# Kernel optimization log

Measured on AMD Instinct MI355X. Metric: run time of the kernel, lower is better.

The kernel has to match this reference:

```python
import jax, jax.numpy as jnp
import numpy as np

K = 16          # neighbors per center (init arg K)
EPS = 1e-5      # layernorm epsilon


def _dcconv(pos, ch, W, b, n_in, n_out, resnet_in=None, Wres=None, bres=None):
    """KNN-gathered distance-contained conv.
    pos: [B, n_in, 3], ch: [B, n_in, Cin], W: [Cout, K, Cin].
    Selects n_out strided centers, gathers K nearest neighbors, convolves.
    """
    stride = n_in // n_out
    idx = jnp.arange(n_out) * stride                      # static center indices
    cpos = pos[:, idx]                                    # [B, n_out, 3]
    # squared pairwise distances centers -> all points: [B, n_out, n_in]
    d2 = jnp.sum((cpos[:, :, None, :] - pos[:, None, :, :]) ** 2, axis=-1)
    _, knn = jax.lax.top_k(-d2, K)                        # [B, n_out, K]
    gathered = jax.vmap(lambda c, i: c[i])(ch, knn)       # [B, n_out, K, Cin]
    out = jnp.einsum('bnkc,okc->bno', gathered, W) + b    # [B, n_out, Cout]
    if resnet_in is None:
        res = ch[:, idx] @ Wres + bres                    # project skip to Cout
    else:
        res = resnet_in[:, idx]                           # downsample carried skip
    return cpos, out, res


def _layernorm(x, g, b):
    mu = jnp.mean(x, axis=-1, keepdims=True)
    var = jnp.var(x, axis=-1, keepdims=True)
    return (x - mu) * jax.lax.rsqrt(var + EPS) * g + b


def setup_inputs() -> dict:
    key = jax.random.key(0)
    ks = jax.random.split(key, 8)
    B, N, Cin, Cout = 2, 8192, 64, 128
    s1 = (2.0 / (K * Cin)) ** 0.5
    s2 = (2.0 / (K * Cout)) ** 0.5
    return {
        'position_matrix': jax.random.normal(ks[0], (B, N, 3), jnp.float32),
        'channel_matrix': jax.random.normal(ks[1], (B, N, Cin), jnp.float32),
        'W1': jax.random.normal(ks[2], (Cout, K, Cin), jnp.float32) * s1,
        'b1': jnp.full((Cout,), 0.01, jnp.float32),
        'Wres': jax.random.normal(ks[3], (Cin, Cout), jnp.float32) * (2.0 / Cin) ** 0.5,
        'bres': jnp.full((Cout,), 0.01, jnp.float32),
        'W2': jax.random.normal(ks[4], (Cout, K, Cout), jnp.float32) * s2,
        'b2': jnp.full((Cout,), 0.01, jnp.float32),
        'g1': jnp.ones((Cout,), jnp.float32),
        'be1': jnp.full((Cout,), 0.01, jnp.float32),
        'g2': jnp.ones((Cout,), jnp.float32),
        'be2': jnp.full((Cout,), 0.01, jnp.float32),
        'n0': 8192, 'n1': 4096, 'n2': 2048,
    }


def reference(position_matrix, channel_matrix, W1, b1, Wres, bres, W2, b2,
              g1, be1, g2, be2, n0, n1, n2):
    pos, ch, res = _dcconv(position_matrix, channel_matrix, W1, b1, n0, n1,
                           None, Wres, bres)
    ch = jax.nn.silu(_layernorm(ch, g1, be1))   # dropout=identity (eval)
    pos, ch, res = _dcconv(pos, ch, W2, b2, n1, n2, resnet_in=res)
    ch = jax.nn.silu(_layernorm(ch, g2, be2))   # dropout=identity (eval)
    ch = ch + res                               # residual add
    return pos, ch
```

## Files before the change

### kernel.cpp

```cpp
#include <hip/hip_runtime.h>
#include <cstdint>
#include <cstddef>

using u16 = unsigned short;
using u32 = unsigned int;
using u64 = unsigned long long;

typedef short bf16x8 __attribute__((ext_vector_type(8)));
typedef float f32x4 __attribute__((ext_vector_type(4)));

constexpr int BATCH = 2;
constexpr int N0 = 8192;
constexpr int N1 = 4096;
constexpr int N2 = 2048;
constexpr int COUT = 128;
constexpr int KNB = 16;

__device__ __forceinline__ float bf2f(u16 v) { return __uint_as_float(((u32)v) << 16); }
__device__ __forceinline__ u16 f2bf(float f) {
    u32 u = __float_as_uint(f);
    return (u16)((u + 0x7fffu + ((u >> 16) & 1u)) >> 16);
}
__device__ __forceinline__ void cvt8(const float* __restrict__ src, u16* __restrict__ dst, int e) {
    float t0[8];
    *(float4*)t0 = *(const float4*)(src + e);
    *(float4*)(t0 + 4) = *(const float4*)(src + e + 4);
    u16 o[8];
#pragma unroll
    for (int q = 0; q < 8; ++q) o[q] = f2bf(t0[q]);
    *(uint4*)(dst + e) = *(uint4*)o;
}

__device__ __forceinline__ float dist2s(float cx, float cy, float cz,
                                        float px, float py, float pz) {
#pragma clang fp contract(off)
    float dx = cx - px;
    float dy = cy - py;
    float dz = cz - pz;
    float s = dx * dx;
    s = s + dy * dy;
    s = s + dz * dz;
    return s;
}

template <int CTRL>
__device__ __forceinline__ u64 dpp64(u64 v) {
    int lo = (int)(u32)v, hi = (int)(u32)(v >> 32);
    int plo = __builtin_amdgcn_update_dpp(0, lo, CTRL, 0xF, 0xF, true);
    int phi = __builtin_amdgcn_update_dpp(0, hi, CTRL, 0xF, 0xF, true);
    return (((u64)(u32)phi) << 32) | (u32)plo;
}
__device__ __forceinline__ u64 dpp_prev_u64(u64 v) { return dpp64<0x111>(v); }

__device__ __forceinline__ void knn_scan(const float* __restrict__ P, int pstride,
                                         int c0row, int c1row, int cnt,
                                         int lane, u64& rk0, u64& rk1) {
    const float* c0p = P + (size_t)c0row * pstride;
    const float* c1p = P + (size_t)c1row * pstride;
    float c0x = c0p[0], c0y = c0p[1], c0z = c0p[2];
    float c1x = c1p[0], c1y = c1p[1], c1z = c1p[2];

    u64 key0, key1;
    {
        const float* pp = P + (size_t)lane * pstride;
        float px = pp[0], py = pp[1], pz = pp[2];
        u64 k0 = (((u64)__float_as_uint(dist2s(c0x, c0y, c0z, px, py, pz))) << 32) | (u32)lane;
        u64 k1 = (((u64)__float_as_uint(dist2s(c1x, c1y, c1z, px, py, pz))) << 32) | (u32)lane;
#pragma unroll
        for (int kk = 2; kk <= 64; kk <<= 1)
#pragma unroll
            for (int jj = kk >> 1; jj > 0; jj >>= 1) {
                u64 o0, o1;
                if (jj == 1)      { o0 = dpp64<0xB1>(k0);  o1 = dpp64<0xB1>(k1); }
                else if (jj == 2) { o0 = dpp64<0x4E>(k0);  o1 = dpp64<0x4E>(k1); }
                else if (jj == 8) { o0 = dpp64<0x128>(k0); o1 = dpp64<0x128>(k1); }
                else              { o0 = __shfl_xor(k0, jj, 64); o1 = __shfl_xor(k1, jj, 64); }
                bool keepmin = (((lane & jj) == 0) == ((lane & kk) == 0));
                k0 = keepmin ? ((o0 < k0) ? o0 : k0) : ((o0 > k0) ? o0 : k0);
                k1 = keepmin ? ((o1 < k1) ? o1 : k1) : ((o1 > k1) ? o1 : k1);
            }
        key0 = k0; key1 = k1;
    }
    u32 cut0 = __shfl((u32)(key0 >> 32), 15, 64);
    u32 cut1 = __shfl((u32)(key1 >> 32), 15, 64);

    {
        const float* pp = P + (size_t)(64 + lane) * pstride;
        float px = pp[0], py = pp[1], pz = pp[2];
        u32 d0 = __float_as_uint(dist2s(c0x, c0y, c0z, px, py, pz));
        u32 d1 = __float_as_uint(dist2s(c1x, c1y, c1z, px, py, pz));
        u64 ball0 = __ballot(d0 <= cut0);
        u64 ball1 = __ballot(d1 <= cut1);
        bool any0 = ball0 != 0, any1 = ball1 != 0;
        while (ball0 | ball1) {
            if (ball0) {
                int src = __ffsll((unsigned long long)ball0) - 1;
                ball0 &= ball0 - 1;
                u64 nk = (((u64)__shfl(d0, src, 64)) << 32) | (u32)(64 + src);
                u64 prev = dpp_prev_u64(key0);
                key0 = (nk < key0) ? ((nk < prev) ? prev : nk) : key0;
            }
            if (ball1) {
                int src = __ffsll((unsigned long long)ball1) - 1;
                ball1 &= ball1 - 1;
                u64 nk = (((u64)__shfl(d1, src, 64)) << 32) | (u32)(64 + src);
                u64 prev = dpp_prev_u64(key1);
                key1 = (nk < key1) ? ((nk < prev) ? prev : nk) : key1;
            }
        }
        if (any0) cut0 = __shfl((u32)(key0 >> 32), 15, 64);
        if (any1) cut1 = __shfl((u32)(key1 >> 32), 15, 64);
    }

    int nstep = (cnt - 128) >> 7;
    const float* pa = P + (size_t)(128 + 2 * lane) * pstride;
    float ax = pa[0], ay = pa[1], az = pa[2];
    float bx = pa[pstride], by = pa[pstride + 1], bz = pa[pstride + 2];
    for (int s = 0; s < nstep; ++s) {
        float cax = ax, cay = ay, caz = az, cbx = bx, cby = by, cbz = bz;
        int nxt = (s + 1 < nstep) ? (s + 1) : s;
        const float* pn = P + (size_t)(128 + (nxt << 7) + 2 * lane) * pstride;
        ax = pn[0]; ay = pn[1]; az = pn[2];
        bx = pn[pstride]; by = pn[pstride + 1]; bz = pn[pstride + 2];
        int sb = 128 + (s << 7);
        u32 da0 = __float_as_uint(dist2s(c0x, c0y, c0z, cax, cay, caz));
        u32 da1 = __float_as_uint(dist2s(c1x, c1y, c1z, cax, cay, caz));
        u32 db0 = __float_as_uint(dist2s(c0x, c0y, c0z, cbx, cby, cbz));
        u32 db1 = __float_as_uint(dist2s(c1x, c1y, c1z, cbx, cby, cbz));
        u64 ba0 = __ballot(da0 <= cut0);
        u64 bb0 = __ballot(db0 <= cut0);
        u64 ba1 = __ballot(da1 <= cut1);
        u64 bb1 = __ballot(db1 <= cut1);
        bool any0 = (ba0 | bb0) != 0, any1 = (ba1 | bb1) != 0;
        while (ba0 | bb0 | ba1 | bb1) {
            if (ba0) {
                int src = __ffsll((unsigned long long)ba0) - 1;
                ba0 &= ba0 - 1;
                u64 nk = (((u64)__shfl(da0, src, 64)) << 32) | (u32)(sb + 2 * src);
                u64 prev = dpp_prev_u64(key0);
                key0 = (nk < key0) ? ((nk < prev) ? prev : nk) : key0;
            }
            if (ba1) {
                int src = __ffsll((unsigned long long)ba1) - 1;
                ba1 &= ba1 - 1;
                u64 nk = (((u64)__shfl(da1, src, 64)) << 32) | (u32)(sb + 2 * src);
                u64 prev = dpp_prev_u64(key1);
                key1 = (nk < key1) ? ((nk < prev) ? prev : nk) : key1;
            }
            if (bb0) {
                int src = __ffsll((unsigned long long)bb0) - 1;
                bb0 &= bb0 - 1;
                u64 nk = (((u64)__shfl(db0, src, 64)) << 32) | (u32)(sb + 2 * src + 1);
                u64 prev = dpp_prev_u64(key0);
                key0 = (nk < key0) ? ((nk < prev) ? prev : nk) : key0;
            }
            if (bb1) {
                int src = __ffsll((unsigned long long)bb1) - 1;
                bb1 &= bb1 - 1;
                u64 nk = (((u64)__shfl(db1, src, 64)) << 32) | (u32)(sb + 2 * src + 1);
                u64 prev = dpp_prev_u64(key1);
                key1 = (nk < key1) ? ((nk < prev) ? prev : nk) : key1;
            }
        }
        if (any0) cut0 = __shfl((u32)(key0 >> 32), 15, 64);
        if (any1) cut1 = __shfl((u32)(key1 >> 32), 15, 64);
    }
    rk0 = key0; rk1 = key1;
}

__global__ __launch_bounds__(256)
void knn_prep_kernel(const float* __restrict__ pos0, const float* __restrict__ ch0,
                     const float* __restrict__ W1, const float* __restrict__ W2,
                     const float* __restrict__ Wres,
                     int* __restrict__ knn1, int* __restrict__ knn2,
                     u16* __restrict__ ch0b, u16* __restrict__ W1b,
                     u16* __restrict__ W2b, u16* __restrict__ Wresb,
                     float* __restrict__ pos_out) {
    int blk = blockIdx.x, tid = threadIdx.x;
    int w = tid >> 6, lane = tid & 63;
    if (blk < 1024) {
        int wave = blk * 4 + w;
        int batch = wave >> 11, pj = wave & 2047;
        const float* P = pos0 + (size_t)batch * N0 * 3;
        u64 key0, key1;
        knn_scan(P, 3, 4 * pj, 4 * pj + 2, N0, lane, key0, key1);
        if (lane < 16) {
            knn1[((size_t)(batch * N1 + 2 * pj)) * KNB + lane] = (int)(u32)key0;
            knn1[((size_t)(batch * N1 + 2 * pj + 1)) * KNB + lane] = (int)(u32)key1;
        }
    } else if (blk < 1536) {
        int wave = (blk - 1024) * 4 + w;
        int batch = wave >> 10, pj = wave & 1023;
        const float* P = pos0 + (size_t)batch * N0 * 3;
        u64 key0, key1;
        knn_scan(P, 6, 4 * pj, 4 * pj + 2, N1, lane, key0, key1);
        if (lane < 16) {
            knn2[((size_t)(batch * N2 + 2 * pj)) * KNB + lane] = (int)(u32)key0;
            knn2[((size_t)(batch * N2 + 2 * pj + 1)) * KNB + lane] = (int)(u32)key1;
        }
    } else if (blk < 2048) {
        cvt8(ch0, ch0b, ((blk - 1536) * 256 + tid) * 8);
    } else if (blk < 2112) {
        cvt8(W1, W1b, ((blk - 2048) * 256 + tid) * 8);
    } else if (blk < 2240) {
        cvt8(W2, W2b, ((blk - 2112) * 256 + tid) * 8);
    } else if (blk < 2272) {
        int t = (blk - 2240) * 256 + tid;
        int o = t >> 6, c = t & 63;
        Wresb[o * 64 + c] = f2bf(Wres[(size_t)c * COUT + o]);
    } else {
        int t = (blk - 2272) * 256 + tid;
        int b = t >> 11, r = t & 2047;
        const float* s = pos0 + ((size_t)(b * N0 + r * 4)) * 3;
        float* d = pos_out + ((size_t)(b * N2 + r)) * 3;
        d[0] = s[0]; d[1] = s[1]; d[2] = s[2];
    }
}

__global__ __launch_bounds__(256)
void conv1_kernel(const u16* __restrict__ ch0b, const int* __restrict__ knn1,
                  const u16* __restrict__ W1b, const u16* __restrict__ Wresb,
                  const float* __restrict__ b1, const float* __restrict__ bres,
                  const float* __restrict__ g1, const float* __restrict__ be1,
                  u16* __restrict__ ch1b, u16* __restrict__ res1b) {
    __shared__ u16 As[16][72];
    __shared__ u16 Ws[128][72];
    __shared__ int knnr[16][16];
    __shared__ float red[16][4][2];
    __shared__ float cb[128], cg[128], cbe[128], cbr[128];

    int tid = threadIdx.x;
    int blk = blockIdx.x;
    int b = blk >> 8, g = blk & 255;
    int jbase = g * 16;

    if (tid < 128) { cb[tid] = b1[tid]; cg[tid] = g1[tid]; cbe[tid] = be1[tid]; cbr[tid] = bres[tid]; }
    {
        int r = tid >> 4, k = tid & 15;
        knnr[r][k] = knn1[((size_t)(b * N1 + jbase + r)) * KNB + k];
    }
    __syncthreads();

    int w = tid >> 6, lane = tid & 63, quad = lane >> 4, l15 = lane & 15;
    int wcol = w * 32;
    int ar = tid >> 4, ap = tid & 15;
    int wn = tid >> 1, wh = tid & 1;

    f32x4 acc[2] = {{0,0,0,0},{0,0,0,0}};
    f32x4 racc[2] = {{0,0,0,0},{0,0,0,0}};

    uint2 aR = *((const uint2*)(ch0b + ((size_t)(b * N0 + knnr[ar][0])) * 64) + ap);
    uint4 wR[4];
    {
        const uint4* s4 = (const uint4*)(W1b + (size_t)wn * 1024 + wh * 32);
        wR[0] = s4[0]; wR[1] = s4[1]; wR[2] = s4[2]; wR[3] = s4[3];
    }
    for (int kn = 0; kn < 17; ++kn) {
        *(uint2*)&As[ar][ap * 4] = aR;
        uint4* d4 = (uint4*)&Ws[wn][wh * 32];
        d4[0] = wR[0]; d4[1] = wR[1]; d4[2] = wR[2]; d4[3] = wR[3];
        __syncthreads();
        if (kn < 16) {
            int nidx = (kn < 15) ? knnr[ar][kn + 1] : 2 * (jbase + ar);
            aR = *((const uint2*)(ch0b + ((size_t)(b * N0 + nidx)) * 64) + ap);
            const uint4* s4 = (kn < 15)
                ? (const uint4*)(W1b + (size_t)wn * 1024 + (kn + 1) * 64 + wh * 32)
                : (const uint4*)(Wresb + (size_t)wn * 64 + wh * 32);
            wR[0] = s4[0]; wR[1] = s4[1]; wR[2] = s4[2]; wR[3] = s4[3];
        }
        if (kn < 16) {
#pragma unroll
            for (int ks = 0; ks < 2; ++ks) {
                bf16x8 af = *(const bf16x8*)&As[l15][ks * 32 + quad * 8];
#pragma unroll
                for (int nt = 0; nt < 2; ++nt) {
                    bf16x8 bfr = *(const bf16x8*)&Ws[wcol + nt * 16 + l15][ks * 32 + quad * 8];
                    acc[nt] = __builtin_amdgcn_mfma_f32_16x16x32_bf16(af, bfr, acc[nt], 0, 0, 0);
                }
            }
        } else {
#pragma unroll
            for (int ks = 0; ks < 2; ++ks) {
                bf16x8 af = *(const bf16x8*)&As[l15][ks * 32 + quad * 8];
#pragma unroll
                for (int nt = 0; nt < 2; ++nt) {
                    bf16x8 bfr = *(const bf16x8*)&Ws[wcol + nt * 16 + l15][ks * 32 + quad * 8];
                    racc[nt] = __builtin_amdgcn_mfma_f32_16x16x32_bf16(af, bfr, racc[nt], 0, 0, 0);
                }
            }
        }
        __syncthreads();
    }

    float x[2][4], s[4] = {0,0,0,0}, ss[4] = {0,0,0,0};
#pragma unroll
    for (int reg = 0; reg < 4; ++reg)
#pragma unroll
        for (int nt = 0; nt < 2; ++nt) {
            int col = wcol + nt * 16 + l15;
            float v = acc[nt][reg] + cb[col];
            x[nt][reg] = v;
            s[reg] += v; ss[reg] += v * v;
        }
#pragma unroll
    for (int m = 1; m < 16; m <<= 1)
#pragma unroll
        for (int reg = 0; reg < 4; ++reg) {
            s[reg] += __shfl_xor(s[reg], m, 64);
            ss[reg] += __shfl_xor(ss[reg], m, 64);
        }
    if (l15 == 0) {
#pragma unroll
        for (int reg = 0; reg < 4; ++reg) {
            red[quad * 4 + reg][w][0] = s[reg];
            red[quad * 4 + reg][w][1] = ss[reg];
        }
    }
    __syncthreads();
    float mu[4], rs[4];
#pragma unroll
    for (int reg = 0; reg < 4; ++reg) {
        int row = quad * 4 + reg;
        float S = red[row][0][0] + red[row][1][0] + red[row][2][0] + red[row][3][0];
        float SS = red[row][0][1] + red[row][1][1] + red[row][2][1] + red[row][3][1];
        mu[reg] = S * (1.f / 128.f);
        float var = fmaxf(SS * (1.f / 128.f) - mu[reg] * mu[reg], 0.f);
        rs[reg] = 1.f / sqrtf(var + 1e-5f);
    }
#pragma unroll
    for (int nt = 0; nt < 2; ++nt)
#pragma unroll
        for (int reg = 0; reg < 4; ++reg) {
            int col = wcol + nt * 16 + l15;
            int row = quad * 4 + reg;
            size_t off = ((size_t)(b * N1 + jbase + row)) * COUT + col;
            float y = (x[nt][reg] - mu[reg]) * rs[reg] * cg[col] + cbe[col];
            ch1b[off] = f2bf(y / (1.f + __expf(-y)));
            res1b[off] = f2bf(racc[nt][reg] + cbr[col]);
        }
}

__global__ __launch_bounds__(512)
void conv2_kernel(const u16* __restrict__ ch1b, const int* __restrict__ knn2,
                  const u16* __restrict__ W2b, const float* __restrict__ b2,
                  const float* __restrict__ g2, const float* __restrict__ be2,
                  const u16* __restrict__ res1b, float* __restrict__ ch_out) {
    __shared__ u16 As[16][136];
    __shared__ u16 Ws[128][136];
    __shared__ int knnr[16][16];
    __shared__ float red[16][8][2];
    __shared__ float cb[128], cg[128], cbe[128];

    int tid = threadIdx.x;
    int b = blockIdx.x >> 7, g = blockIdx.x & 127;
    int ibase = g * 16;

    if (tid < 128) { cb[tid] = b2[tid]; cg[tid] = g2[tid]; cbe[tid] = be2[tid]; }
    if (tid < 256) {
        int r = tid >> 4, k = tid & 15;
        knnr[r][k] = knn2[((size_t)(b * N2 + ibase + r)) * KNB + k];
    }
    __syncthreads();

    int w = tid >> 6, lane = tid & 63, quad = lane >> 4, l15 = lane & 15;
    int wcol = w * 16;
    int ar = tid >> 5, ap = tid & 31;
    int wn = tid >> 2, wq = tid & 3;

    f32x4 acc = {0, 0, 0, 0};

    uint2 aR = *((const uint2*)(ch1b + ((size_t)(b * N1 + knnr[ar][0])) * COUT) + ap);
    uint4 wR[4];
    {
        const uint4* s4 = (const uint4*)(W2b + (size_t)wn * 2048 + wq * 32);
        wR[0] = s4[0]; wR[1] = s4[1]; wR[2] = s4[2]; wR[3] = s4[3];
    }
    for (int kn = 0; kn < 16; ++kn) {
        *(uint2*)&As[ar][ap * 4] = aR;
        uint4* d4 = (uint4*)&Ws[wn][wq * 32];
        d4[0] = wR[0]; d4[1] = wR[1]; d4[2] = wR[2]; d4[3] = wR[3];
        __syncthreads();
        if (kn < 15) {
            aR = *((const uint2*)(ch1b + ((size_t)(b * N1 + knnr[ar][kn + 1])) * COUT) + ap);
            const uint4* s4 = (const uint4*)(W2b + (size_t)wn * 2048 + (kn + 1) * 128 + wq * 32);
            wR[0] = s4[0]; wR[1] = s4[1]; wR[2] = s4[2]; wR[3] = s4[3];
        }
#pragma unroll
        for (int ks = 0; ks < 4; ++ks) {
            bf16x8 af = *(const bf16x8*)&As[l15][ks * 32 + quad * 8];
            bf16x8 bfr = *(const bf16x8*)&Ws[wcol + l15][ks * 32 + quad * 8];
            acc = __builtin_amdgcn_mfma_f32_16x16x32_bf16(af, bfr, acc, 0, 0, 0);
        }
        __syncthreads();
    }

    float x[4], s[4], ss[4];
#pragma unroll
    for (int reg = 0; reg < 4; ++reg) {
        int col = wcol + l15;
        float v = acc[reg] + cb[col];
        x[reg] = v; s[reg] = v; ss[reg] = v * v;
    }
#pragma unroll
    for (int m = 1; m < 16; m <<= 1)
#pragma unroll
        for (int reg = 0; reg < 4; ++reg) {
            s[reg] += __shfl_xor(s[reg], m, 64);
            ss[reg] += __shfl_xor(ss[reg], m, 64);
        }
    if (l15 == 0) {
#pragma unroll
        for (int reg = 0; reg < 4; ++reg) {
            red[quad * 4 + reg][w][0] = s[reg];
            red[quad * 4 + reg][w][1] = ss[reg];
        }
    }
    __syncthreads();
#pragma unroll
    for (int reg = 0; reg < 4; ++reg) {
        int row = quad * 4 + reg;
        float S = 0.f, SS = 0.f;
#pragma unroll
        for (int t = 0; t < 8; ++t) { S += red[row][t][0]; SS += red[row][t][1]; }
        float mu = S * (1.f / 128.f);
        float var = fmaxf(SS * (1.f / 128.f) - mu * mu, 0.f);
        float rs = 1.f / sqrtf(var + 1e-5f);
        int col = wcol + l15;
        int i = ibase + row;
        float y = (x[reg] - mu) * rs * cg[col] + cbe[col];
        float sl = y / (1.f + __expf(-y));
        float rv = bf2f(res1b[((size_t)(b * N1 + 2 * i)) * COUT + col]);
        ch_out[((size_t)(b * N2 + i)) * COUT + col] = sl + rv;
    }
}

extern "C" void kernel_launch(void* const* d_in, const int* in_sizes, int n_in,
                              void* d_out, int out_size, void* d_ws, size_t ws_size,
                              hipStream_t stream) {
    const float* pos0 = (const float*)d_in[0];
    const float* ch0  = (const float*)d_in[1];
    const float* W1   = (const float*)d_in[2];
    const float* b1   = (const float*)d_in[3];
    const float* Wres = (const float*)d_in[4];
    const float* bres = (const float*)d_in[5];
    const float* W2   = (const float*)d_in[6];
    const float* b2   = (const float*)d_in[7];
    const float* g1   = (const float*)d_in[8];
    const float* be1  = (const float*)d_in[9];
    const float* g2   = (const float*)d_in[10];
    const float* be2  = (const float*)d_in[11];
    float* out = (float*)d_out;

    char* ws = (char*)d_ws;
    int*  knn1  = (int*)(ws);
    int*  knn2  = (int*)(ws + 524288);
    u16*  ch0b  = (u16*)(ws + 786432);
    u16*  W1b   = (u16*)(ws + 2883584);
    u16*  W2b   = (u16*)(ws + 3145728);
    u16*  Wresb = (u16*)(ws + 3670016);
    u16*  ch1b  = (u16*)(ws + 3686400);
    u16*  res1b = (u16*)(ws + 5783552);

    float* pos_out = out;
    float* ch_out  = out + 12288;

    knn_prep_kernel<<<2288, 256, 0, stream>>>(pos0, ch0, W1, W2, Wres,
                                              knn1, knn2, ch0b, W1b, W2b, Wresb, pos_out);
    conv1_kernel<<<512, 256, 0, stream>>>(ch0b, knn1, W1b, Wresb, b1, bres, g1, be1, ch1b, res1b);
    conv2_kernel<<<256, 512, 0, stream>>>(ch1b, knn2, W2b, b2, g2, be2, res1b, ch_out);
}
```

Before: 225.0 us.

## Move second KNN search into conv1 launch and use readlane for broadcasts

The second-level KNN search moves out of the prep kernel and into the conv1 kernel as extra blocks, so it overlaps with the first convolution instead of extending the prep kernel's long tail. Inside the scan, wave-uniform broadcasts switch from __shfl (LDS bpermute) to readlane, the point stride becomes a template parameter, and the conditional cut refresh becomes unconditional. This spreads KNN work across two launches but makes the conv1 launch heterogeneous, which can affect scheduling and occupancy.

```diff
diff --git a/kernel.cpp b/kernel.cpp
--- a/kernel.cpp
+++ b/kernel.cpp
@@ -9,7 +9,6 @@
 typedef short bf16x8 __attribute__((ext_vector_type(8)));
 typedef float f32x4 __attribute__((ext_vector_type(4)));
 
-constexpr int BATCH = 2;
 constexpr int N0 = 8192;
 constexpr int N1 = 4096;
 constexpr int N2 = 2048;
@@ -52,17 +51,22 @@
 }
 __device__ __forceinline__ u64 dpp_prev_u64(u64 v) { return dpp64<0x111>(v); }
 
-__device__ __forceinline__ void knn_scan(const float* __restrict__ P, int pstride,
+__device__ __forceinline__ u32 rdlane(u32 v, int l) {
+    return (u32)__builtin_amdgcn_readlane((int)v, l);
+}
+
+template <int PSTRIDE>
+__device__ __forceinline__ void knn_scan(const float* __restrict__ P,
                                          int c0row, int c1row, int cnt,
                                          int lane, u64& rk0, u64& rk1) {
-    const float* c0p = P + (size_t)c0row * pstride;
-    const float* c1p = P + (size_t)c1row * pstride;
+    const float* c0p = P + (size_t)c0row * PSTRIDE;
+    const float* c1p = P + (size_t)c1row * PSTRIDE;
     float c0x = c0p[0], c0y = c0p[1], c0z = c0p[2];
     float c1x = c1p[0], c1y = c1p[1], c1z = c1p[2];
 
     u64 key0, key1;
     {
-        const float* pp = P + (size_t)lane * pstride;
+        const float* pp = P + (size_t)lane * PSTRIDE;
         float px = pp[0], py = pp[1], pz = pp[2];
         u64 k0 = (((u64)__float_as_uint(dist2s(c0x, c0y, c0z, px, py, pz))) << 32) | (u32)lane;
         u64 k1 = (((u64)__float_as_uint(dist2s(c1x, c1y, c1z, px, py, pz))) << 32) | (u32)lane;
@@ -81,47 +85,48 @@
             }
         key0 = k0; key1 = k1;
     }
-    u32 cut0 = __shfl((u32)(key0 >> 32), 15, 64);
-    u32 cut1 = __shfl((u32)(key1 >> 32), 15, 64);
+    u32 cut0 = rdlane((u32)(key0 >> 32), 15);
+    u32 cut1 = rdlane((u32)(key1 >> 32), 15);
 
     {
-        const float* pp = P + (size_t)(64 + lane) * pstride;
+        const float* pp = P + (size_t)(64 + lane) * PSTRIDE;
         float px = pp[0], py = pp[1], pz = pp[2];
         u32 d0 = __float_as_uint(dist2s(c0x, c0y, c0z, px, py, pz));
         u32 d1 = __float_as_uint(dist2s(c1x, c1y, c1z, px, py, pz));
         u64 ball0 = __ballot(d0 <= cut0);
         u64 ball1 = __ballot(d1 <= cut1);
-        bool any0 = ball0 != 0, any1 = ball1 != 0;
         while (ball0 | ball1) {
             if (ball0) {
                 int src = __ffsll((unsigned long long)ball0) - 1;
                 ball0 &= ball0 - 1;
-                u64 nk = (((u64)__shfl(d0, src, 64)) << 32) | (u32)(64 + src);
+                u64 nk = (((u64)rdlane(d0, src)) << 32) | (u32)(64 + src);
                 u64 prev = dpp_prev_u64(key0);
                 key0 = (nk < key0) ? ((nk < prev) ? prev : nk) : key0;
             }
             if (ball1) {
                 int src = __ffsll((unsigned long long)ball1) - 1;
                 ball1 &= ball1 - 1;
-                u64 nk = (((u64)__shfl(d1, src, 64)) << 32) | (u32)(64 + src);
+                u64 nk = (((u64)rdlane(d1, src)) << 32) | (u32)(64 + src);
                 u64 prev = dpp_prev_u64(key1);
                 key1 = (nk < key1) ? ((nk < prev) ? prev : nk) : key1;
             }
         }
-        if (any0) cut0 = __shfl((u32)(key0 >> 32), 15, 64);
-        if (any1) cut1 = __shfl((u32)(key1 >> 32), 15, 64);
-    }
-
+        cut0 = rdlane((u32)(key0 >> 32), 15);
+        cut1 = rdlane((u32)(key1 >> 32), 15);
+    }
+
+    constexpr int STEPF = 128 * PSTRIDE;
     int nstep = (cnt - 128) >> 7;
-    const float* pa = P + (size_t)(128 + 2 * lane) * pstride;
-    float ax = pa[0], ay = pa[1], az = pa[2];
-    float bx = pa[pstride], by = pa[pstride + 1], bz = pa[pstride + 2];
+    const float* cur = P + (size_t)(128 + 2 * lane) * PSTRIDE;
+    float ax = cur[0], ay = cur[1], az = cur[2];
+    float bx = cur[PSTRIDE], by = cur[PSTRIDE + 1], bz = cur[PSTRIDE + 2];
     for (int s = 0; s < nstep; ++s) {
         float cax = ax, cay = ay, caz = az, cbx = bx, cby = by, cbz = bz;
-        int nxt = (s + 1 < nstep) ? (s + 1) : s;
-        const float* pn = P + (size_t)(128 + (nxt << 7) + 2 * lane) * pstride;
-        ax = pn[0]; ay = pn[1]; az = pn[2];
-        bx = pn[pstride]; by = pn[pstride + 1]; bz = pn[pstride + 2];
+        cur += STEPF;
+        if (s + 1 < nstep) {
+            ax = cur[0]; ay = cur[1]; az = cur[2];
+            bx = cur[PSTRIDE]; by = cur[PSTRIDE + 1]; bz = cur[PSTRIDE + 2];
+        }
         int sb = 128 + (s << 7);
         u32 da0 = __float_as_uint(dist2s(c0x, c0y, c0z, cax, cay, caz));
         u32 da1 = __float_as_uint(dist2s(c1x, c1y, c1z, cax, cay, caz));
@@ -131,39 +136,38 @@
         u64 bb0 = __ballot(db0 <= cut0);
         u64 ba1 = __ballot(da1 <= cut1);
         u64 bb1 = __ballot(db1 <= cut1);
-        bool any0 = (ba0 | bb0) != 0, any1 = (ba1 | bb1) != 0;
         while (ba0 | bb0 | ba1 | bb1) {
             if (ba0) {
                 int src = __ffsll((unsigned long long)ba0) - 1;
                 ba0 &= ba0 - 1;
-                u64 nk = (((u64)__shfl(da0, src, 64)) << 32) | (u32)(sb + 2 * src);
+                u64 nk = (((u64)rdlane(da0, src)) << 32) | (u32)(sb + 2 * src);
                 u64 prev = dpp_prev_u64(key0);
                 key0 = (nk < key0) ? ((nk < prev) ? prev : nk) : key0;
             }
             if (ba1) {
                 int src = __ffsll((unsigned long long)ba1) - 1;
                 ba1 &= ba1 - 1;
-                u64 nk = (((u64)__shfl(da1, src, 64)) << 32) | (u32)(sb + 2 * src);
+                u64 nk = (((u64)rdlane(da1, src)) << 32) | (u32)(sb + 2 * src);
                 u64 prev = dpp_prev_u64(key1);
                 key1 = (nk < key1) ? ((nk < prev) ? prev : nk) : key1;
             }
             if (bb0) {
                 int src = __ffsll((unsigned long long)bb0) - 1;
                 bb0 &= bb0 - 1;
-                u64 nk = (((u64)__shfl(db0, src, 64)) << 32) | (u32)(sb + 2 * src + 1);
+                u64 nk = (((u64)rdlane(db0, src)) << 32) | (u32)(sb + 2 * src + 1);
                 u64 prev = dpp_prev_u64(key0);
                 key0 = (nk < key0) ? ((nk < prev) ? prev : nk) : key0;
             }
             if (bb1) {
                 int src = __ffsll((unsigned long long)bb1) - 1;
                 bb1 &= bb1 - 1;
-                u64 nk = (((u64)__shfl(db1, src, 64)) << 32) | (u32)(sb + 2 * src + 1);
+                u64 nk = (((u64)rdlane(db1, src)) << 32) | (u32)(sb + 2 * src + 1);
                 u64 prev = dpp_prev_u64(key1);
                 key1 = (nk < key1) ? ((nk < prev) ? prev : nk) : key1;
             }
         }
-        if (any0) cut0 = __shfl((u32)(key0 >> 32), 15, 64);
-        if (any1) cut1 = __shfl((u32)(key1 >> 32), 15, 64);
+        cut0 = rdlane((u32)(key0 >> 32), 15);
+        cut1 = rdlane((u32)(key1 >> 32), 15);
     }
     rk0 = key0; rk1 = key1;
 }
@@ -172,7 +176,7 @@
 void knn_prep_kernel(const float* __restrict__ pos0, const float* __restrict__ ch0,
                      const float* __restrict__ W1, const float* __restrict__ W2,
                      const float* __restrict__ Wres,
-                     int* __restrict__ knn1, int* __restrict__ knn2,
+                     int* __restrict__ knn1,
                      u16* __restrict__ ch0b, u16* __restrict__ W1b,
                      u16* __restrict__ W2b, u16* __restrict__ Wresb,
                      float* __restrict__ pos_out) {
@@ -183,33 +187,23 @@
         int batch = wave >> 11, pj = wave & 2047;
         const float* P = pos0 + (size_t)batch * N0 * 3;
         u64 key0, key1;
-        knn_scan(P, 3, 4 * pj, 4 * pj + 2, N0, lane, key0, key1);
+        knn_scan<3>(P, 4 * pj, 4 * pj + 2, N0, lane, key0, key1);
         if (lane < 16) {
             knn1[((size_t)(batch * N1 + 2 * pj)) * KNB + lane] = (int)(u32)key0;
             knn1[((size_t)(batch * N1 + 2 * pj + 1)) * KNB + lane] = (int)(u32)key1;
         }
     } else if (blk < 1536) {
-        int wave = (blk - 1024) * 4 + w;
-        int batch = wave >> 10, pj = wave & 1023;
-        const float* P = pos0 + (size_t)batch * N0 * 3;
-        u64 key0, key1;
-        knn_scan(P, 6, 4 * pj, 4 * pj + 2, N1, lane, key0, key1);
-        if (lane < 16) {
-            knn2[((size_t)(batch * N2 + 2 * pj)) * KNB + lane] = (int)(u32)key0;
-            knn2[((size_t)(batch * N2 + 2 * pj + 1)) * KNB + lane] = (int)(u32)key1;
-        }
-    } else if (blk < 2048) {
-        cvt8(ch0, ch0b, ((blk - 1536) * 256 + tid) * 8);
-    } else if (blk < 2112) {
-        cvt8(W1, W1b, ((blk - 2048) * 256 + tid) * 8);
-    } else if (blk < 2240) {
-        cvt8(W2, W2b, ((blk - 2112) * 256 + tid) * 8);
-    } else if (blk < 2272) {
-        int t = (blk - 2240) * 256 + tid;
+        cvt8(ch0, ch0b, ((blk - 1024) * 256 + tid) * 8);
+    } else if (blk < 1600) {
+        cvt8(W1, W1b, ((blk - 1536) * 256 + tid) * 8);
+    } else if (blk < 1728) {
+        cvt8(W2, W2b, ((blk - 1600) * 256 + tid) * 8);
+    } else if (blk < 1760) {
+        int t = (blk - 1728) * 256 + tid;
         int o = t >> 6, c = t & 63;
         Wresb[o * 64 + c] = f2bf(Wres[(size_t)c * COUT + o]);
     } else {
-        int t = (blk - 2272) * 256 + tid;
+        int t = (blk - 1760) * 256 + tid;
         int b = t >> 11, r = t & 2047;
         const float* s = pos0 + ((size_t)(b * N0 + r * 4)) * 3;
         float* d = pos_out + ((size_t)(b * N2 + r)) * 3;
@@ -218,20 +212,36 @@
 }
 
 __global__ __launch_bounds__(256)
-void conv1_kernel(const u16* __restrict__ ch0b, const int* __restrict__ knn1,
-                  const u16* __restrict__ W1b, const u16* __restrict__ Wresb,
-                  const float* __restrict__ b1, const float* __restrict__ bres,
-                  const float* __restrict__ g1, const float* __restrict__ be1,
-                  u16* __restrict__ ch1b, u16* __restrict__ res1b) {
+void conv1_knn2_kernel(const u16* __restrict__ ch0b, const int* __restrict__ knn1,
+                       const u16* __restrict__ W1b, const u16* __restrict__ Wresb,
+                       const float* __restrict__ b1, const float* __restrict__ bres,
+                       const float* __restrict__ g1, const float* __restrict__ be1,
+                       u16* __restrict__ ch1b, u16* __restrict__ res1b,
+                       const float* __restrict__ pos0, int* __restrict__ knn2) {
     __shared__ u16 As[16][72];
     __shared__ u16 Ws[128][72];
     __shared__ int knnr[16][16];
     __shared__ float red[16][4][2];
     __shared__ float cb[128], cg[128], cbe[128], cbr[128];
 
-    int tid = threadIdx.x;
-    int blk = blockIdx.x;
-    int b = blk >> 8, g = blk & 255;
+    int blk = blockIdx.x, tid = threadIdx.x;
+
+    if (blk < 512) {
+        int w = tid >> 6, lane = tid & 63;
+        int wave = blk * 4 + w;
+        int batch = wave >> 10, pj = wave & 1023;
+        const float* P = pos0 + (size_t)batch * N0 * 3;
+        u64 key0, key1;
+        knn_scan<6>(P, 4 * pj, 4 * pj + 2, N1, lane, key0, key1);
+        if (lane < 16) {
+            knn2[((size_t)(batch * N2 + 2 * pj)) * KNB + lane] = (int)(u32)key0;
+            knn2[((size_t)(batch * N2 + 2 * pj + 1)) * KNB + lane] = (int)(u32)key1;
+        }
+        return;
+    }
+
+    int cblk = blk - 512;
+    int b = cblk >> 8, g = cblk & 255;
     int jbase = g * 16;
 
     if (tid < 128) { cb[tid] = b1[tid]; cg[tid] = g1[tid]; cbe[tid] = be1[tid]; cbr[tid] = bres[tid]; }
@@ -464,8 +474,9 @@
     float* pos_out = out;
     float* ch_out  = out + 12288;
 
-    knn_prep_kernel<<<2288, 256, 0, stream>>>(pos0, ch0, W1, W2, Wres,
-                                              knn1, knn2, ch0b, W1b, W2b, Wresb, pos_out);
-    conv1_kernel<<<512, 256, 0, stream>>>(ch0b, knn1, W1b, Wresb, b1, bres, g1, be1, ch1b, res1b);
+    knn_prep_kernel<<<1776, 256, 0, stream>>>(pos0, ch0, W1, W2, Wres,
+                                              knn1, ch0b, W1b, W2b, Wresb, pos_out);
+    conv1_knn2_kernel<<<1024, 256, 0, stream>>>(ch0b, knn1, W1b, Wresb, b1, bres, g1, be1,
+                                                ch1b, res1b, pos0, knn2);
     conv2_kernel<<<256, 512, 0, stream>>>(ch1b, knn2, W2b, b2, g2, be2, res1b, ch_out);
 }
```

Measured after the change: 221.3 us. About the same (-1.6%).
